# Optimization experiments

Measured on AMD Instinct MI355X. Metric: run time of the kernel, lower is better.

Reference implementation:

```python
import math
import jax, jax.numpy as jnp
import numpy as np

B, S, HID = 2, 2048, 3072
NH, HD = 32, 96            # num_heads, head_dim; num_kv_heads == num_heads (n_rep = 1)
OP = NH * HD + 2 * (NH * HD)  # 9216


def _rope_tables(seq_len, head_dim, theta=10000.0):
    inv_freq = 1.0 / (theta ** (np.arange(0, head_dim, 2, dtype=np.float32) / head_dim))
    t = np.arange(seq_len, dtype=np.float32)
    freqs = np.outer(t, inv_freq)                      # [S, HD/2]
    emb = np.concatenate([freqs, freqs], axis=-1)      # [S, HD]
    return jnp.asarray(np.cos(emb)), jnp.asarray(np.sin(emb))


def setup_inputs() -> dict:
    key = jax.random.key(0)
    k1, k2, k3 = jax.random.split(key, 3)
    hidden_states = jax.random.normal(k1, (B, S, HID), dtype=jnp.float32)
    cos, sin = _rope_tables(S, HD)
    # additive causal mask [B, 1, S, S]
    neg = jnp.finfo(jnp.float32).min
    causal = jnp.where(jnp.tril(jnp.ones((S, S), dtype=bool)), 0.0, neg)
    attention_mask = jnp.broadcast_to(causal[None, None], (B, 1, S, S)).astype(jnp.float32)
    Wqkv = jax.random.normal(k2, (HID, OP), dtype=jnp.float32) * (HID ** -0.5)
    Wo = jax.random.normal(k3, (NH * HD, HID), dtype=jnp.float32) * ((NH * HD) ** -0.5)
    return {"hidden_states": hidden_states, "cos": cos, "sin": sin,
            "attention_mask": attention_mask, "Wqkv": Wqkv, "Wo": Wo}


def _rotate_half(x):
    x1, x2 = jnp.split(x, 2, axis=-1)
    return jnp.concatenate([-x2, x1], axis=-1)


def reference(hidden_states, cos, sin, attention_mask, Wqkv, Wo):
    bsz, q_len, _ = hidden_states.shape
    qkv = hidden_states @ Wqkv                                    # [B,S,OP]
    q, k, v = jnp.split(qkv, [NH * HD, 2 * NH * HD], axis=-1)
    # [B,S,H*D] -> [B,H,S,D]
    to_bhsd = lambda t: t.reshape(bsz, q_len, NH, HD).transpose(0, 2, 1, 3)
    q, k, v = to_bhsd(q), to_bhsd(k), to_bhsd(v)
    c = cos[None, None]                                           # [1,1,S,D]
    s = sin[None, None]
    q = q * c + _rotate_half(q) * s
    k = k * c + _rotate_half(k) * s
    # num_key_value_groups == 1, so repeat_kv is identity.
    scores = jnp.einsum('bhqd,bhkd->bhqk', q, k) / math.sqrt(HD)  # [B,H,S,S]
    scores = scores + attention_mask
    attn = jax.nn.softmax(scores.astype(jnp.float32), axis=-1).astype(v.dtype)
    # dropout p=0.0 / eval -> identity
    out = jnp.einsum('bhqk,bhkd->bhqd', attn, v)                  # [B,H,S,D]
    out = out.transpose(0, 2, 1, 3).reshape(bsz, q_len, NH * HD)
    return out @ Wo                                               # [B,S,HID]
```

## Files before the change

### kernel.cpp

```cpp
#include <hip/hip_runtime.h>

typedef __bf16  bf16x8 __attribute__((ext_vector_type(8)));
typedef float   f32x4  __attribute__((ext_vector_type(4)));
typedef short   i16x8  __attribute__((ext_vector_type(8)));
typedef unsigned short u16x4 __attribute__((ext_vector_type(4)));

__device__ __forceinline__ float bf2f(unsigned short u) {
    union { unsigned int i; float f; } v; v.i = ((unsigned int)u) << 16; return v.f;
}
__device__ __forceinline__ unsigned short f2bf(float f) {
    union { float f; unsigned int i; } v; v.f = f;
    unsigned int r = v.i + 0x7FFFu + ((v.i >> 16) & 1u);
    return (unsigned short)(r >> 16);
}
__device__ __forceinline__ void gload_lds16(const void* g, void* l) {
    __builtin_amdgcn_global_load_lds(
        (const __attribute__((address_space(1))) void*)g,
        (__attribute__((address_space(3))) void*)l, 16, 0, 0);
}

__global__ __launch_bounds__(256) void cast_f32_bf16(
    const float* __restrict__ in, unsigned short* __restrict__ out, int n8)
{
    int i = blockIdx.x * 256 + threadIdx.x;
    if (i >= n8) return;
    const f32x4* p = (const f32x4*)(in + (long)i * 8);
    f32x4 a = p[0], b = p[1];
    i16x8 o;
    o[0]=(short)f2bf(a[0]); o[1]=(short)f2bf(a[1]); o[2]=(short)f2bf(a[2]); o[3]=(short)f2bf(a[3]);
    o[4]=(short)f2bf(b[0]); o[5]=(short)f2bf(b[1]); o[6]=(short)f2bf(b[2]); o[7]=(short)f2bf(b[3]);
    *(i16x8*)(out + (long)i * 8) = o;
}

__global__ __launch_bounds__(256) void transpose_cast(
    const float* __restrict__ in, unsigned short* __restrict__ out, int R, int C)
{
    __shared__ float tile[64][65];
    int c0 = blockIdx.x * 64, r0 = blockIdx.y * 64;
    int tx = threadIdx.x & 63, ty = threadIdx.x >> 6;
#pragma unroll
    for (int i = 0; i < 64; i += 4)
        tile[ty + i][tx] = in[(long)(r0 + ty + i) * C + c0 + tx];
    __syncthreads();
#pragma unroll
    for (int i = 0; i < 64; i += 4)
        out[(long)(c0 + ty + i) * R + r0 + tx] = f2bf(tile[tx][ty + i]);
}

template <int MODE>
__global__ __launch_bounds__(256) void gemm_bt(
    const unsigned short* __restrict__ A, const unsigned short* __restrict__ B,
    int K, int N,
    unsigned short* __restrict__ Qo, unsigned short* __restrict__ Ko,
    unsigned short* __restrict__ Vo, float* __restrict__ Cf)
{
    __shared__ unsigned short Al[128 * 64];
    __shared__ unsigned short Bl[128 * 64];
    const int t = threadIdx.x;
    const int w = t >> 6, l = t & 63, lhi = l >> 4, llo = l & 15;
    const int m0 = blockIdx.x * 128, n0 = blockIdx.y * 128;
    const int wmo = (w >> 1) << 6, wno = (w & 1) << 6;

    const unsigned short* ag[4];
    const unsigned short* bg[4];
#pragma unroll
    for (int i = 0; i < 4; ++i) {
        int j = i * 256 + t;
        int row = j >> 3;
        int c = (j & 7) ^ (row & 7);
        ag[i] = A + (long)(m0 + row) * K + c * 8;
        bg[i] = B + (long)(n0 + row) * K + c * 8;
    }

    f32x4 acc[4][4] = {};
    const int nkt = K >> 6;
    for (int kt = 0; kt < nkt; ++kt) {
        __syncthreads();
#pragma unroll
        for (int i = 0; i < 4; ++i) {
            gload_lds16(ag[i] + kt * 64, &Al[(i * 256 + (w << 6)) * 8]);
            gload_lds16(bg[i] + kt * 64, &Bl[(i * 256 + (w << 6)) * 8]);
        }
        __syncthreads();
#pragma unroll
        for (int kf = 0; kf < 2; ++kf) {
            bf16x8 af[4], bfv[4];
#pragma unroll
            for (int mi = 0; mi < 4; ++mi) {
                int row = wmo + mi * 16 + llo;
                int cc = (kf * 4 + lhi) ^ (row & 7);
                af[mi] = __builtin_bit_cast(bf16x8, *(const i16x8*)&Al[row * 64 + cc * 8]);
            }
#pragma unroll
            for (int ni = 0; ni < 4; ++ni) {
                int row = wno + ni * 16 + llo;
                int cc = (kf * 4 + lhi) ^ (row & 7);
                bfv[ni] = __builtin_bit_cast(bf16x8, *(const i16x8*)&Bl[row * 64 + cc * 8]);
            }
#pragma unroll
            for (int mi = 0; mi < 4; ++mi)
#pragma unroll
                for (int ni = 0; ni < 4; ++ni)
                    acc[mi][ni] = __builtin_amdgcn_mfma_f32_16x16x32_bf16(
                        af[mi], bfv[ni], acc[mi][ni], 0, 0, 0);
        }
    }

#pragma unroll
    for (int mi = 0; mi < 4; ++mi) {
        int s0g = m0 + wmo + mi * 16 + (lhi << 2);
#pragma unroll
        for (int ni = 0; ni < 4; ++ni) {
            int gcol = n0 + wno + ni * 16 + llo;
            if (MODE == 1) {
#pragma unroll
                for (int r = 0; r < 4; ++r)
                    Cf[(long)(s0g + r) * N + gcol] = acc[mi][ni][r];
            } else {
                int seg = gcol / 3072;
                int cc2 = gcol - seg * 3072;
                int h = cc2 / 96, d = cc2 - h * 96;
                int b = s0g >> 11, s = s0g & 2047;
                long bh = (long)((b << 5) + h);
                if (seg == 2) {
                    u16x4 pv;
#pragma unroll
                    for (int r = 0; r < 4; ++r) pv[r] = f2bf(acc[mi][ni][r]);
                    *(u16x4*)(Vo + (bh * 96 + d) * 2048 + s) = pv;
                } else {
                    unsigned short* dst = seg ? Ko : Qo;
#pragma unroll
                    for (int r = 0; r < 4; ++r)
                        dst[(bh * 2048 + s + r) * 96 + d] = f2bf(acc[mi][ni][r]);
                }
            }
        }
    }
}

__global__ __launch_bounds__(256) void rope_kernel(
    unsigned short* __restrict__ Qb, unsigned short* __restrict__ Kb,
    const float* __restrict__ cosT, const float* __restrict__ sinT)
{
    int i = blockIdx.x * 256 + threadIdx.x;
    int d6 = i % 6;
    int sbh = i / 6;
    int s = sbh & 2047;
    long base = (long)sbh * 96 + d6 * 8;
    const f32x4* cp = (const f32x4*)(cosT + s * 96 + d6 * 8);
    const f32x4* sp = (const f32x4*)(sinT + s * 96 + d6 * 8);
    f32x4 c0 = cp[0], c1 = cp[1], s0 = sp[0], s1 = sp[1];
    float cv[8] = {c0[0],c0[1],c0[2],c0[3],c1[0],c1[1],c1[2],c1[3]};
    float sv[8] = {s0[0],s0[1],s0[2],s0[3],s1[0],s1[1],s1[2],s1[3]};
    i16x8 qlo = *(i16x8*)(Qb + base), qhi = *(i16x8*)(Qb + base + 48);
    i16x8 klo = *(i16x8*)(Kb + base), khi = *(i16x8*)(Kb + base + 48);
    i16x8 qlo2, qhi2, klo2, khi2;
#pragma unroll
    for (int j = 0; j < 8; ++j) {
        float ql = bf2f((unsigned short)qlo[j]), qh = bf2f((unsigned short)qhi[j]);
        float kl = bf2f((unsigned short)klo[j]), kh = bf2f((unsigned short)khi[j]);
        qlo2[j] = (short)f2bf(ql * cv[j] - qh * sv[j]);
        qhi2[j] = (short)f2bf(qh * cv[j] + ql * sv[j]);
        klo2[j] = (short)f2bf(kl * cv[j] - kh * sv[j]);
        khi2[j] = (short)f2bf(kh * cv[j] + kl * sv[j]);
    }
    *(i16x8*)(Qb + base) = qlo2; *(i16x8*)(Qb + base + 48) = qhi2;
    *(i16x8*)(Kb + base) = klo2; *(i16x8*)(Kb + base + 48) = khi2;
}

__global__ __launch_bounds__(256, 3) void attn_fwd(
    const unsigned short* __restrict__ Q, const unsigned short* __restrict__ Kt,
    const unsigned short* __restrict__ Vg, unsigned short* __restrict__ O)
{
    __shared__ unsigned short Kl[64 * 104];
    __shared__ unsigned short Vl[96 * 72];
    __shared__ unsigned short Pl[4][16 * 88];
    const int t = threadIdx.x;
    const int w = t >> 6, l = t & 63, lhi = l >> 4, llo = l & 15;
    const int bx = blockIdx.x, bh = blockIdx.y;
    constexpr float C2 = 0.14724450f;

    int klds[3], vlds[3];
    const unsigned short* kg[3];
    const unsigned short* vg[3];
#pragma unroll
    for (int i = 0; i < 3; ++i) {
        int c = t + i * 256;
        int srow = c / 12, scc = c % 12;
        kg[i] = Kt + ((long)bh * 2048 + srow) * 96 + scc * 8;
        klds[i] = srow * 104 + scc * 8;
        int vrow = c >> 3, vch = c & 7;
        vg[i] = Vg + ((long)bh * 96 + vrow) * 2048 + vch * 8;
        vlds[i] = vrow * 72 + vch * 8;
    }

    const int b = bh >> 5, h = bh & 31;

    for (int pass = 0; pass < 2; ++pass) {
        const int qb = pass ? (31 - bx) : bx;
        const int q0 = qb << 6;

        bf16x8 qf[3];
        {
            const unsigned short* qp =
                Q + ((long)bh * 2048 + q0 + (w << 4) + llo) * 96 + (lhi << 3);
#pragma unroll
            for (int kf = 0; kf < 3; ++kf)
                qf[kf] = __builtin_bit_cast(bf16x8, *(const i16x8*)(qp + kf * 32));
        }

        f32x4 oacc[6] = {};
        float m_r[4] = {-1e30f, -1e30f, -1e30f, -1e30f};
        float l_l[4] = {0.f, 0.f, 0.f, 0.f};

        i16x8 kreg[3], vreg[3];
#pragma unroll
        for (int i = 0; i < 3; ++i) {
            kreg[i] = *(const i16x8*)kg[i];
            vreg[i] = *(const i16x8*)vg[i];
        }

        for (int kt = 0; kt <= qb; ++kt) {
            __syncthreads();
#pragma unroll
            for (int i = 0; i < 3; ++i) {
                *(i16x8*)&Kl[klds[i]] = kreg[i];
                *(i16x8*)&Vl[vlds[i]] = vreg[i];
            }
            __syncthreads();
            if (kt < qb) {
#pragma unroll
                for (int i = 0; i < 3; ++i) {
                    kreg[i] = *(const i16x8*)(kg[i] + (long)(kt + 1) * 64 * 96);
                    vreg[i] = *(const i16x8*)(vg[i] + (kt + 1) * 64);
                }
            }

            f32x4 sa[4] = {};
#pragma unroll
            for (int kf = 0; kf < 3; ++kf) {
#pragma unroll
                for (int nf = 0; nf < 4; ++nf) {
                    bf16x8 bfr = __builtin_bit_cast(bf16x8,
                        *(const i16x8*)&Kl[(nf * 16 + llo) * 104 + kf * 32 + (lhi << 3)]);
                    sa[nf] = __builtin_amdgcn_mfma_f32_16x16x32_bf16(qf[kf], bfr, sa[nf], 0, 0, 0);
                }
            }
            if (kt == qb) {
#pragma unroll
                for (int nf = 0; nf < 4; ++nf) {
                    int col = nf * 16 + llo;
#pragma unroll
                    for (int r = 0; r < 4; ++r)
                        if (col > (w << 4) + (lhi << 2) + r) sa[nf][r] = -1e30f;
                }
            }

#pragma unroll
            for (int r = 0; r < 4; ++r) {
                float mx = fmaxf(fmaxf(sa[0][r], sa[1][r]), fmaxf(sa[2][r], sa[3][r]));
                mx = fmaxf(mx, __shfl_xor(mx, 1));
                mx = fmaxf(mx, __shfl_xor(mx, 2));
                mx = fmaxf(mx, __shfl_xor(mx, 4));
                mx = fmaxf(mx, __shfl_xor(mx, 8));
                if (__any(mx > m_r[r] + 54.0f)) {
                    float mnew = fmaxf(m_r[r], mx);
                    float scl = exp2f((m_r[r] - mnew) * C2);
                    l_l[r] *= scl;
#pragma unroll
                    for (int nf = 0; nf < 6; ++nf) oacc[nf][r] *= scl;
                    m_r[r] = mnew;
                }
                float mC = m_r[r] * C2;
                float rs = 0.f;
#pragma unroll
                for (int nf = 0; nf < 4; ++nf) {
                    float p = exp2f(fmaf(sa[nf][r], C2, -mC));
                    rs += p;
                    Pl[w][((lhi << 2) + r) * 88 + nf * 16 + llo] = f2bf(p);
                }
                l_l[r] += rs;
            }

#pragma unroll
            for (int kf = 0; kf < 2; ++kf) {
                bf16x8 pa = __builtin_bit_cast(bf16x8,
                    *(const i16x8*)&Pl[w][llo * 88 + kf * 32 + (lhi << 3)]);
#pragma unroll
                for (int nf = 0; nf < 6; ++nf) {
                    bf16x8 bv = __builtin_bit_cast(bf16x8,
                        *(const i16x8*)&Vl[(nf * 16 + llo) * 72 + kf * 32 + (lhi << 3)]);
                    oacc[nf] = __builtin_amdgcn_mfma_f32_16x16x32_bf16(pa, bv, oacc[nf], 0, 0, 0);
                }
            }
        }

#pragma unroll
        for (int r = 0; r < 4; ++r) {
            float s = l_l[r];
            s += __shfl_xor(s, 1);
            s += __shfl_xor(s, 2);
            s += __shfl_xor(s, 4);
            s += __shfl_xor(s, 8);
            float inv = 1.0f / s;
            long ob = ((long)(b * 2048 + q0 + (w << 4) + (lhi << 2) + r)) * 3072 + h * 96;
#pragma unroll
            for (int nf = 0; nf < 6; ++nf)
                O[ob + nf * 16 + llo] = f2bf(oacc[nf][r] * inv);
        }
    }
}

extern "C" void kernel_launch(void* const* d_in, const int* in_sizes, int n_in,
                              void* d_out, int out_size, void* d_ws, size_t ws_size,
                              hipStream_t stream) {
    const float* hidden = (const float*)d_in[0];
    const float* cosT   = (const float*)d_in[1];
    const float* sinT   = (const float*)d_in[2];
    const float* Wqkv   = (const float*)d_in[4];
    const float* Wo     = (const float*)d_in[5];
    float* out = (float*)d_out;

    char* ws = (char*)d_ws;
    unsigned short* Ah  = (unsigned short*)ws;
    unsigned short* WqT = (unsigned short*)(ws + 25165824);
    unsigned short* Qb  = (unsigned short*)(ws + 25165824 + 56623104);
    unsigned short* Kb  = Qb + 12582912;
    unsigned short* Vb  = Kb + 12582912;

    cast_f32_bf16<<<6144, 256, 0, stream>>>(hidden, Ah, 1572864);
    transpose_cast<<<dim3(144, 48), 256, 0, stream>>>(Wqkv, WqT, 3072, 9216);
    gemm_bt<0><<<dim3(32, 72), 256, 0, stream>>>(Ah, WqT, 3072, 9216, Qb, Kb, Vb, nullptr);
    transpose_cast<<<dim3(48, 48), 256, 0, stream>>>(Wo, WqT, 3072, 3072);
    rope_kernel<<<3072, 256, 0, stream>>>(Qb, Kb, cosT, sinT);
    attn_fwd<<<dim3(16, 64), 256, 0, stream>>>(Qb, Kb, Vb, Ah);
    gemm_bt<1><<<dim3(32, 24), 256, 0, stream>>>(Ah, WqT, 3072, 3072,
                                                 nullptr, nullptr, nullptr, out);
}
```

Measured before the change: 560.6 us.

## Replace GEMM with 256x256 double-buffered tile kernel and XCD-aware block remap

Swaps the 128x128 single-buffered bf16 GEMM for a 256x256-tile, 512-thread kernel. It double-buffers LDS with global_load_lds prefetch two K-steps ahead, using vmcnt waits and split barriers, and raises MFMA priority with s_setprio. Blocks are remapped across the 8 XCDs for cache locality. The aim is to hide global-load latency and raise arithmetic intensity for the QKV and output projections, at the cost of 128KB of LDS and fewer workgroups (576 and 192), which hurts occupancy and tail balance on the smaller GEMM.

```diff
diff --git a/kernel.cpp b/kernel.cpp
--- a/kernel.cpp
+++ b/kernel.cpp
@@ -48,70 +48,110 @@
 }
 
 template <int MODE>
-__global__ __launch_bounds__(256) void gemm_bt(
+__global__ __launch_bounds__(512, 2) void gemm256(
     const unsigned short* __restrict__ A, const unsigned short* __restrict__ B,
-    int K, int N,
+    int K, int N, int nbx,
     unsigned short* __restrict__ Qo, unsigned short* __restrict__ Ko,
     unsigned short* __restrict__ Vo, float* __restrict__ Cf)
 {
-    __shared__ unsigned short Al[128 * 64];
-    __shared__ unsigned short Bl[128 * 64];
+    __shared__ __align__(16) unsigned short As[2][256 * 64];
+    __shared__ __align__(16) unsigned short Bs[2][256 * 64];
     const int t = threadIdx.x;
-    const int w = t >> 6, l = t & 63, lhi = l >> 4, llo = l & 15;
-    const int m0 = blockIdx.x * 128, n0 = blockIdx.y * 128;
-    const int wmo = (w >> 1) << 6, wno = (w & 1) << 6;
-
-    const unsigned short* ag[4];
-    const unsigned short* bg[4];
+    const int w = t >> 6, l = t & 63, lhi = (l >> 4), llo = l & 15;
+    const int wm = w >> 2, wn = w & 3;
+
+    const int nwg = gridDim.x, cpx = nwg >> 3;
+    const int wg = ((int)blockIdx.x & 7) * cpx + ((int)blockIdx.x >> 3);
+    const int bx = wg % nbx, by = wg / nbx;
+    const int m0 = bx << 8, n0 = by << 8;
+
+    const unsigned short* aG[4];
+    const unsigned short* bG[4];
+    int ldsOff[4];
 #pragma unroll
     for (int i = 0; i < 4; ++i) {
-        int j = i * 256 + t;
+        int j = i * 512 + t;
         int row = j >> 3;
         int c = (j & 7) ^ (row & 7);
-        ag[i] = A + (long)(m0 + row) * K + c * 8;
-        bg[i] = B + (long)(n0 + row) * K + c * 8;
-    }
-
-    f32x4 acc[4][4] = {};
+        aG[i] = A + (long)(m0 + row) * K + c * 8;
+        bG[i] = B + (long)(n0 + row) * K + c * 8;
+        ldsOff[i] = (i * 512 + (w << 6)) * 8;
+    }
+
     const int nkt = K >> 6;
+#pragma unroll
+    for (int i = 0; i < 4; ++i) {
+        gload_lds16(aG[i], &As[0][ldsOff[i]]);
+        gload_lds16(bG[i], &Bs[0][ldsOff[i]]);
+    }
+#pragma unroll
+    for (int i = 0; i < 4; ++i) {
+        gload_lds16(aG[i] + 64, &As[1][ldsOff[i]]);
+        gload_lds16(bG[i] + 64, &Bs[1][ldsOff[i]]);
+    }
+
+    f32x4 acc[8][4] = {};
+
     for (int kt = 0; kt < nkt; ++kt) {
-        __syncthreads();
-#pragma unroll
-        for (int i = 0; i < 4; ++i) {
-            gload_lds16(ag[i] + kt * 64, &Al[(i * 256 + (w << 6)) * 8]);
-            gload_lds16(bg[i] + kt * 64, &Bl[(i * 256 + (w << 6)) * 8]);
-        }
-        __syncthreads();
-#pragma unroll
-        for (int kf = 0; kf < 2; ++kf) {
-            bf16x8 af[4], bfv[4];
-#pragma unroll
-            for (int mi = 0; mi < 4; ++mi) {
-                int row = wmo + mi * 16 + llo;
-                int cc = (kf * 4 + lhi) ^ (row & 7);
-                af[mi] = __builtin_bit_cast(bf16x8, *(const i16x8*)&Al[row * 64 + cc * 8]);
-            }
-#pragma unroll
-            for (int ni = 0; ni < 4; ++ni) {
-                int row = wno + ni * 16 + llo;
-                int cc = (kf * 4 + lhi) ^ (row & 7);
-                bfv[ni] = __builtin_bit_cast(bf16x8, *(const i16x8*)&Bl[row * 64 + cc * 8]);
-            }
-#pragma unroll
-            for (int mi = 0; mi < 4; ++mi)
-#pragma unroll
-                for (int ni = 0; ni < 4; ++ni)
-                    acc[mi][ni] = __builtin_amdgcn_mfma_f32_16x16x32_bf16(
-                        af[mi], bfv[ni], acc[mi][ni], 0, 0, 0);
-        }
-    }
-
-#pragma unroll
-    for (int mi = 0; mi < 4; ++mi) {
-        int s0g = m0 + wmo + mi * 16 + (lhi << 2);
+        const int c = kt & 1;
+        if (kt < nkt - 1) asm volatile("s_waitcnt vmcnt(8)" ::: "memory");
+        else              asm volatile("s_waitcnt vmcnt(0)" ::: "memory");
+        __builtin_amdgcn_s_barrier();
+
+        const unsigned short* Ab = As[c];
+        const unsigned short* Bb = Bs[c];
+        bf16x8 af[8];
+#pragma unroll
+        for (int kh = 0; kh < 2; ++kh) {
+#pragma unroll
+            for (int mi = 0; mi < 8; ++mi) {
+                int row = (wm << 7) + (mi << 4) + llo;
+                int cc = ((kh << 2) + lhi) ^ (row & 7);
+                af[mi] = __builtin_bit_cast(bf16x8, *(const i16x8*)&Ab[row * 64 + cc * 8]);
+            }
+#pragma unroll
+            for (int nh = 0; nh < 2; ++nh) {
+                bf16x8 b0, b1;
+                {
+                    int row = (wn << 6) + (nh << 5) + llo;
+                    int cc = ((kh << 2) + lhi) ^ (row & 7);
+                    b0 = __builtin_bit_cast(bf16x8, *(const i16x8*)&Bb[row * 64 + cc * 8]);
+                    row += 16;
+                    cc = ((kh << 2) + lhi) ^ (row & 7);
+                    b1 = __builtin_bit_cast(bf16x8, *(const i16x8*)&Bb[row * 64 + cc * 8]);
+                }
+                const bool last = (kh == 1) && (nh == 1);
+                if (last) {
+                    asm volatile("s_waitcnt lgkmcnt(0)" ::: "memory");
+                }
+                __builtin_amdgcn_s_barrier();
+                if (last && (kt + 2 < nkt)) {
+                    const long off = (long)(kt + 2) * 64;
+#pragma unroll
+                    for (int i = 0; i < 4; ++i) {
+                        gload_lds16(aG[i] + off, &As[c][ldsOff[i]]);
+                        gload_lds16(bG[i] + off, &Bs[c][ldsOff[i]]);
+                    }
+                }
+                __builtin_amdgcn_s_setprio(1);
+#pragma unroll
+                for (int mi = 0; mi < 8; ++mi) {
+                    acc[mi][(nh << 1)]     = __builtin_amdgcn_mfma_f32_16x16x32_bf16(
+                        af[mi], b0, acc[mi][(nh << 1)], 0, 0, 0);
+                    acc[mi][(nh << 1) + 1] = __builtin_amdgcn_mfma_f32_16x16x32_bf16(
+                        af[mi], b1, acc[mi][(nh << 1) + 1], 0, 0, 0);
+                }
+                __builtin_amdgcn_s_setprio(0);
+            }
+        }
+    }
+
+#pragma unroll
+    for (int mi = 0; mi < 8; ++mi) {
+        int s0g = m0 + (wm << 7) + (mi << 4) + (lhi << 2);
 #pragma unroll
         for (int ni = 0; ni < 4; ++ni) {
-            int gcol = n0 + wno + ni * 16 + llo;
+            int gcol = n0 + (wn << 6) + (ni << 4) + llo;
             if (MODE == 1) {
 #pragma unroll
                 for (int r = 0; r < 4; ++r)
@@ -330,10 +370,10 @@
 
     cast_f32_bf16<<<6144, 256, 0, stream>>>(hidden, Ah, 1572864);
     transpose_cast<<<dim3(144, 48), 256, 0, stream>>>(Wqkv, WqT, 3072, 9216);
-    gemm_bt<0><<<dim3(32, 72), 256, 0, stream>>>(Ah, WqT, 3072, 9216, Qb, Kb, Vb, nullptr);
+    gemm256<0><<<576, 512, 0, stream>>>(Ah, WqT, 3072, 9216, 16, Qb, Kb, Vb, nullptr);
     transpose_cast<<<dim3(48, 48), 256, 0, stream>>>(Wo, WqT, 3072, 3072);
     rope_kernel<<<3072, 256, 0, stream>>>(Qb, Kb, cosT, sinT);
     attn_fwd<<<dim3(16, 64), 256, 0, stream>>>(Qb, Kb, Vb, Ah);
-    gemm_bt<1><<<dim3(32, 24), 256, 0, stream>>>(Ah, WqT, 3072, 3072,
-                                                 nullptr, nullptr, nullptr, out);
-}
+    gemm256<1><<<192, 512, 0, stream>>>(Ah, WqT, 3072, 3072, 16,
+                                        nullptr, nullptr, nullptr, out);
+}
```

Result: slower. 598.5 us (median of 2 runs) (+6.8%).

## Double attention Q-tile to 128 rows per block, two 16-row MFMA tiles per wave

Applied to the files above, without the earlier changes.

Each attention block now handles 128 query rows instead of 64, with every wave computing two 16-row sub-tiles that share the same K and V fragments read from LDS. This halves the K/V global loads and LDS staging per query row and halves the grid. The causal mask now uses global row and column indices over the last two KV tiles. In exchange, register use roughly doubles (occupancy hint lowered from 3 to 2), there are fewer blocks for load balancing, and a little extra masked work lands on the diagonal tiles.

```diff
diff --git a/kernel.cpp b/kernel.cpp
--- a/kernel.cpp
+++ b/kernel.cpp
@@ -168,13 +168,13 @@
     *(i16x8*)(Kb + base) = klo2; *(i16x8*)(Kb + base + 48) = khi2;
 }
 
-__global__ __launch_bounds__(256, 3) void attn_fwd(
+__global__ __launch_bounds__(256, 2) void attn_fwd(
     const unsigned short* __restrict__ Q, const unsigned short* __restrict__ Kt,
     const unsigned short* __restrict__ Vg, unsigned short* __restrict__ O)
 {
     __shared__ unsigned short Kl[64 * 104];
     __shared__ unsigned short Vl[96 * 72];
-    __shared__ unsigned short Pl[4][16 * 88];
+    __shared__ unsigned short Pl[4][32 * 88];
     const int t = threadIdx.x;
     const int w = t >> 6, l = t & 63, lhi = l >> 4, llo = l & 15;
     const int bx = blockIdx.x, bh = blockIdx.y;
@@ -197,21 +197,23 @@
     const int b = bh >> 5, h = bh & 31;
 
     for (int pass = 0; pass < 2; ++pass) {
-        const int qb = pass ? (31 - bx) : bx;
-        const int q0 = qb << 6;
-
-        bf16x8 qf[3];
-        {
+        const int qb = pass ? (15 - bx) : bx;
+        const int q0 = qb << 7;
+        const int nkv = 2 * qb + 2;
+
+        bf16x8 qf[2][3];
+#pragma unroll
+        for (int mi = 0; mi < 2; ++mi) {
             const unsigned short* qp =
-                Q + ((long)bh * 2048 + q0 + (w << 4) + llo) * 96 + (lhi << 3);
+                Q + ((long)bh * 2048 + q0 + (w << 5) + (mi << 4) + llo) * 96 + (lhi << 3);
 #pragma unroll
             for (int kf = 0; kf < 3; ++kf)
-                qf[kf] = __builtin_bit_cast(bf16x8, *(const i16x8*)(qp + kf * 32));
-        }
-
-        f32x4 oacc[6] = {};
-        float m_r[4] = {-1e30f, -1e30f, -1e30f, -1e30f};
-        float l_l[4] = {0.f, 0.f, 0.f, 0.f};
+                qf[mi][kf] = __builtin_bit_cast(bf16x8, *(const i16x8*)(qp + kf * 32));
+        }
+
+        f32x4 oacc[2][6] = {};
+        float m_r[2][4] = {{-1e30f,-1e30f,-1e30f,-1e30f},{-1e30f,-1e30f,-1e30f,-1e30f}};
+        float l_l[2][4] = {};
 
         i16x8 kreg[3], vreg[3];
 #pragma unroll
@@ -220,7 +222,7 @@
             vreg[i] = *(const i16x8*)vg[i];
         }
 
-        for (int kt = 0; kt <= qb; ++kt) {
+        for (int kt = 0; kt < nkv; ++kt) {
             __syncthreads();
 #pragma unroll
             for (int i = 0; i < 3; ++i) {
@@ -228,7 +230,7 @@
                 *(i16x8*)&Vl[vlds[i]] = vreg[i];
             }
             __syncthreads();
-            if (kt < qb) {
+            if (kt < nkv - 1) {
 #pragma unroll
                 for (int i = 0; i < 3; ++i) {
                     kreg[i] = *(const i16x8*)(kg[i] + (long)(kt + 1) * 64 * 96);
@@ -236,77 +238,96 @@
                 }
             }
 
-            f32x4 sa[4] = {};
+            f32x4 sa[2][4] = {};
 #pragma unroll
             for (int kf = 0; kf < 3; ++kf) {
 #pragma unroll
                 for (int nf = 0; nf < 4; ++nf) {
                     bf16x8 bfr = __builtin_bit_cast(bf16x8,
                         *(const i16x8*)&Kl[(nf * 16 + llo) * 104 + kf * 32 + (lhi << 3)]);
-                    sa[nf] = __builtin_amdgcn_mfma_f32_16x16x32_bf16(qf[kf], bfr, sa[nf], 0, 0, 0);
-                }
-            }
-            if (kt == qb) {
-#pragma unroll
-                for (int nf = 0; nf < 4; ++nf) {
-                    int col = nf * 16 + llo;
-#pragma unroll
-                    for (int r = 0; r < 4; ++r)
-                        if (col > (w << 4) + (lhi << 2) + r) sa[nf][r] = -1e30f;
-                }
-            }
-
+#pragma unroll
+                    for (int mi = 0; mi < 2; ++mi)
+                        sa[mi][nf] = __builtin_amdgcn_mfma_f32_16x16x32_bf16(
+                            qf[mi][kf], bfr, sa[mi][nf], 0, 0, 0);
+                }
+            }
+            if (kt >= 2 * qb) {
+#pragma unroll
+                for (int mi = 0; mi < 2; ++mi)
+#pragma unroll
+                    for (int nf = 0; nf < 4; ++nf) {
+                        int colg = (kt << 6) + nf * 16 + llo;
+#pragma unroll
+                        for (int r = 0; r < 4; ++r) {
+                            int rowg = q0 + (w << 5) + (mi << 4) + (lhi << 2) + r;
+                            if (colg > rowg) sa[mi][nf][r] = -1e30f;
+                        }
+                    }
+            }
+
+#pragma unroll
+            for (int mi = 0; mi < 2; ++mi)
 #pragma unroll
             for (int r = 0; r < 4; ++r) {
-                float mx = fmaxf(fmaxf(sa[0][r], sa[1][r]), fmaxf(sa[2][r], sa[3][r]));
+                float mx = fmaxf(fmaxf(sa[mi][0][r], sa[mi][1][r]),
+                                 fmaxf(sa[mi][2][r], sa[mi][3][r]));
                 mx = fmaxf(mx, __shfl_xor(mx, 1));
                 mx = fmaxf(mx, __shfl_xor(mx, 2));
                 mx = fmaxf(mx, __shfl_xor(mx, 4));
                 mx = fmaxf(mx, __shfl_xor(mx, 8));
-                if (__any(mx > m_r[r] + 54.0f)) {
-                    float mnew = fmaxf(m_r[r], mx);
-                    float scl = exp2f((m_r[r] - mnew) * C2);
-                    l_l[r] *= scl;
-#pragma unroll
-                    for (int nf = 0; nf < 6; ++nf) oacc[nf][r] *= scl;
-                    m_r[r] = mnew;
-                }
-                float mC = m_r[r] * C2;
+                if (__any(mx > m_r[mi][r] + 54.0f)) {
+                    float mnew = fmaxf(m_r[mi][r], mx);
+                    float scl = exp2f((m_r[mi][r] - mnew) * C2);
+                    l_l[mi][r] *= scl;
+#pragma unroll
+                    for (int nf = 0; nf < 6; ++nf) oacc[mi][nf][r] *= scl;
+                    m_r[mi][r] = mnew;
+                }
+                float mC = m_r[mi][r] * C2;
                 float rs = 0.f;
 #pragma unroll
                 for (int nf = 0; nf < 4; ++nf) {
-                    float p = exp2f(fmaf(sa[nf][r], C2, -mC));
+                    float p = exp2f(fmaf(sa[mi][nf][r], C2, -mC));
                     rs += p;
-                    Pl[w][((lhi << 2) + r) * 88 + nf * 16 + llo] = f2bf(p);
-                }
-                l_l[r] += rs;
+                    Pl[w][((mi << 4) + (lhi << 2) + r) * 88 + nf * 16 + llo] = f2bf(p);
+                }
+                l_l[mi][r] += rs;
             }
 
 #pragma unroll
             for (int kf = 0; kf < 2; ++kf) {
-                bf16x8 pa = __builtin_bit_cast(bf16x8,
-                    *(const i16x8*)&Pl[w][llo * 88 + kf * 32 + (lhi << 3)]);
+                bf16x8 pa[2];
+#pragma unroll
+                for (int mi = 0; mi < 2; ++mi)
+                    pa[mi] = __builtin_bit_cast(bf16x8,
+                        *(const i16x8*)&Pl[w][((mi << 4) + llo) * 88 + kf * 32 + (lhi << 3)]);
 #pragma unroll
                 for (int nf = 0; nf < 6; ++nf) {
                     bf16x8 bv = __builtin_bit_cast(bf16x8,
                         *(const i16x8*)&Vl[(nf * 16 + llo) * 72 + kf * 32 + (lhi << 3)]);
-                    oacc[nf] = __builtin_amdgcn_mfma_f32_16x16x32_bf16(pa, bv, oacc[nf], 0, 0, 0);
-                }
-            }
-        }
-
+#pragma unroll
+                    for (int mi = 0; mi < 2; ++mi)
+                        oacc[mi][nf] = __builtin_amdgcn_mfma_f32_16x16x32_bf16(
+                            pa[mi], bv, oacc[mi][nf], 0, 0, 0);
+                }
+            }
+        }
+
+#pragma unroll
+        for (int mi = 0; mi < 2; ++mi)
 #pragma unroll
         for (int r = 0; r < 4; ++r) {
-            float s = l_l[r];
+            float s = l_l[mi][r];
             s += __shfl_xor(s, 1);
             s += __shfl_xor(s, 2);
             s += __shfl_xor(s, 4);
             s += __shfl_xor(s, 8);
             float inv = 1.0f / s;
-            long ob = ((long)(b * 2048 + q0 + (w << 4) + (lhi << 2) + r)) * 3072 + h * 96;
+            long ob = ((long)(b * 2048 + q0 + (w << 5) + (mi << 4) + (lhi << 2) + r)) * 3072
+                      + h * 96;
 #pragma unroll
             for (int nf = 0; nf < 6; ++nf)
-                O[ob + nf * 16 + llo] = f2bf(oacc[nf][r] * inv);
+                O[ob + nf * 16 + llo] = f2bf(oacc[mi][nf][r] * inv);
         }
     }
 }
@@ -333,7 +354,7 @@
     gemm_bt<0><<<dim3(32, 72), 256, 0, stream>>>(Ah, WqT, 3072, 9216, Qb, Kb, Vb, nullptr);
     transpose_cast<<<dim3(48, 48), 256, 0, stream>>>(Wo, WqT, 3072, 3072);
     rope_kernel<<<3072, 256, 0, stream>>>(Qb, Kb, cosT, sinT);
-    attn_fwd<<<dim3(16, 64), 256, 0, stream>>>(Qb, Kb, Vb, Ah);
+    attn_fwd<<<dim3(8, 64), 256, 0, stream>>>(Qb, Kb, Vb, Ah);
     gemm_bt<1><<<dim3(32, 24), 256, 0, stream>>>(Ah, WqT, 3072, 3072,
                                                  nullptr, nullptr, nullptr, out);
 }
```

After: 541.7 us. 3.4% less time.

## Rewrite attention with 32x32 MFMA, register-resident P, and double-buffered async KV staging

Applied to the files above, without the earlier changes.

The attention kernel now gives each block 256 query rows, with each wave owning 64 rows. It computes S^T with 32x32x16 bf16 MFMAs and builds the P operand in registers via permlane32 swaps, so P no longer goes through LDS. K and V tiles are double-buffered in LDS, loaded with global_load_lds into XOR-swizzled layouts, and the heaviest causal blocks are scheduled first. This is meant to cut LDS traffic, synchronisation and per-tile overhead, but it raises register pressure and lowers occupancy to 2 blocks per CU. Waves whose diagonal comes early also sit idle in later tiles.

```diff
diff --git a/kernel.cpp b/kernel.cpp
--- a/kernel.cpp
+++ b/kernel.cpp
@@ -2,8 +2,10 @@
 
 typedef __bf16  bf16x8 __attribute__((ext_vector_type(8)));
 typedef float   f32x4  __attribute__((ext_vector_type(4)));
+typedef float   f32x16 __attribute__((ext_vector_type(16)));
 typedef short   i16x8  __attribute__((ext_vector_type(8)));
 typedef unsigned short u16x4 __attribute__((ext_vector_type(4)));
+typedef unsigned int   u32x4 __attribute__((ext_vector_type(4)));
 
 __device__ __forceinline__ float bf2f(unsigned short u) {
     union { unsigned int i; float f; } v; v.i = ((unsigned int)u) << 16; return v.f;
@@ -13,10 +15,28 @@
     unsigned int r = v.i + 0x7FFFu + ((v.i >> 16) & 1u);
     return (unsigned short)(r >> 16);
 }
+__device__ __forceinline__ unsigned packbf(float lo, float hi) {
+    return (unsigned)f2bf(lo) | ((unsigned)f2bf(hi) << 16);
+}
 __device__ __forceinline__ void gload_lds16(const void* g, void* l) {
     __builtin_amdgcn_global_load_lds(
         (const __attribute__((address_space(1))) void*)g,
         (__attribute__((address_space(3))) void*)l, 16, 0, 0);
+}
+__device__ __forceinline__ void pswap(unsigned &x, unsigned &y) {
+#if __has_builtin(__builtin_amdgcn_permlane32_swap)
+    auto r = __builtin_amdgcn_permlane32_swap((int)x, (int)y, false, false);
+    x = (unsigned)r[0]; y = (unsigned)r[1];
+#else
+    unsigned nx = (threadIdx.x & 32) ? (unsigned)__shfl_xor((int)y, 32) : x;
+    unsigned ny = (threadIdx.x & 32) ? y : (unsigned)__shfl_xor((int)x, 32);
+    x = nx; y = ny;
+#endif
+}
+__device__ __forceinline__ float partner_f(float v, int hi) {
+    unsigned x = __builtin_bit_cast(unsigned, v), y = x;
+    pswap(x, y);
+    return __builtin_bit_cast(float, hi ? x : y);
 }
 
 __global__ __launch_bounds__(256) void cast_f32_bf16(
@@ -168,146 +188,158 @@
     *(i16x8*)(Kb + base) = klo2; *(i16x8*)(Kb + base + 48) = khi2;
 }
 
-__global__ __launch_bounds__(256, 3) void attn_fwd(
+__global__ __launch_bounds__(256, 2) void attn_fwd(
     const unsigned short* __restrict__ Q, const unsigned short* __restrict__ Kt,
     const unsigned short* __restrict__ Vg, unsigned short* __restrict__ O)
 {
-    __shared__ unsigned short Kl[64 * 104];
-    __shared__ unsigned short Vl[96 * 72];
-    __shared__ unsigned short Pl[4][16 * 88];
+    __shared__ __align__(16) unsigned short Kl[2][64 * 128];
+    __shared__ __align__(16) unsigned short Vl[2][96 * 64];
     const int t = threadIdx.x;
-    const int w = t >> 6, l = t & 63, lhi = l >> 4, llo = l & 15;
-    const int bx = blockIdx.x, bh = blockIdx.y;
+    const int w = t >> 6, l = t & 63;
+    const int l31 = l & 31, hi = l >> 5, l7 = l & 7;
+    const int bh = blockIdx.x;
+    const int qb = 7 - (int)blockIdx.y;
+    const int q0b = qb << 8;
+    const int nkv = 4 * qb + 4;
+    const int kd = 4 * qb + w;
     constexpr float C2 = 0.14724450f;
 
-    int klds[3], vlds[3];
-    const unsigned short* kg[3];
-    const unsigned short* vg[3];
-#pragma unroll
-    for (int i = 0; i < 3; ++i) {
-        int c = t + i * 256;
-        int srow = c / 12, scc = c % 12;
-        kg[i] = Kt + ((long)bh * 2048 + srow) * 96 + scc * 8;
-        klds[i] = srow * 104 + scc * 8;
-        int vrow = c >> 3, vch = c & 7;
-        vg[i] = Vg + ((long)bh * 96 + vrow) * 2048 + vch * 8;
-        vlds[i] = vrow * 72 + vch * 8;
-    }
+    const unsigned short* Kg  = Kt + (long)bh * 2048 * 96;
+    const unsigned short* Vgb = Vg + (long)bh * 96 * 2048;
+
+#define STAGE_KV(buf, tile)                                                        \
+    {                                                                              \
+        _Pragma("unroll")                                                          \
+        for (int i_ = 0; i_ < 4; ++i_) {                                           \
+            int row_ = (w << 4) + (i_ << 2) + (l >> 4);                            \
+            gload_lds16(Kg + ((long)(tile) * 64 + row_) * 96 +                     \
+                            (((l & 15) ^ (row_ & 7)) << 3),                        \
+                        &Kl[buf][((w << 4) + (i_ << 2)) << 7]);                    \
+        }                                                                          \
+        _Pragma("unroll")                                                          \
+        for (int i_ = 0; i_ < 3; ++i_) {                                           \
+            int row_ = w * 24 + (i_ << 3) + (l >> 3);                              \
+            gload_lds16(Vgb + (long)row_ * 2048 + (tile) * 64 +                    \
+                            ((l7 ^ (row_ & 7)) << 3),                              \
+                        &Vl[buf][(w * 24 + (i_ << 3)) << 6]);                      \
+        }                                                                          \
+    }
+
+    bf16x8 qf[2][6];
+#pragma unroll
+    for (int qs = 0; qs < 2; ++qs) {
+        const unsigned short* qp =
+            Q + ((long)bh * 2048 + q0b + (w << 6) + (qs << 5) + l31) * 96 + (hi << 3);
+#pragma unroll
+        for (int ks = 0; ks < 6; ++ks)
+            qf[qs][ks] = __builtin_bit_cast(bf16x8, *(const i16x8*)(qp + ks * 16));
+    }
+
+    f32x16 oa[2][3] = {};
+    float m_r[2] = {-1e30f, -1e30f};
+    float l_r[2] = {0.f, 0.f};
+
+    STAGE_KV(0, 0);
+    __syncthreads();
+    STAGE_KV(1, 1);
+
+    for (int kt = 0; kt < nkv; ++kt) {
+        const int cb = kt & 1;
+        if (kt <= kd) {
+            bf16x8 pf[2][4];
+#pragma unroll
+            for (int qs = 0; qs < 2; ++qs) {
+                f32x16 s0 = {}, s1 = {};
+#pragma unroll
+                for (int ks = 0; ks < 6; ++ks) {
+                    bf16x8 k0 = __builtin_bit_cast(bf16x8, *(const i16x8*)
+                        &Kl[cb][(l31 << 7) + ((((ks << 1) + hi) ^ l7) << 3)]);
+                    bf16x8 k1 = __builtin_bit_cast(bf16x8, *(const i16x8*)
+                        &Kl[cb][((32 + l31) << 7) + ((((ks << 1) + hi) ^ l7) << 3)]);
+                    s0 = __builtin_amdgcn_mfma_f32_32x32x16_bf16(k0, qf[qs][ks], s0, 0, 0, 0);
+                    s1 = __builtin_amdgcn_mfma_f32_32x32x16_bf16(k1, qf[qs][ks], s1, 0, 0, 0);
+                }
+                if (kt == kd) {
+                    const int ql = (qs << 5) + l31;
+#pragma unroll
+                    for (int r = 0; r < 16; ++r) {
+                        int kvl = (r & 3) + ((r >> 2) << 3) + (hi << 2);
+                        if (kvl > ql)      s0[r] = -1e30f;
+                        if (kvl + 32 > ql) s1[r] = -1e30f;
+                    }
+                }
+                float px = s0[0];
+#pragma unroll
+                for (int r = 1; r < 16; ++r) px = fmaxf(px, s0[r]);
+#pragma unroll
+                for (int r = 0; r < 16; ++r) px = fmaxf(px, s1[r]);
+                px = fmaxf(px, partner_f(px, hi));
+                if (__any(px > m_r[qs] + 54.0f)) {
+                    float mnew = fmaxf(m_r[qs], px);
+                    float scl = exp2f((m_r[qs] - mnew) * C2);
+                    l_r[qs] *= scl;
+#pragma unroll
+                    for (int tt = 0; tt < 3; ++tt)
+#pragma unroll
+                        for (int r = 0; r < 16; ++r) oa[qs][tt][r] *= scl;
+                    m_r[qs] = mnew;
+                }
+                const float mC = m_r[qs] * C2;
+                f32x16 p0, p1;
+                float ls = 0.f;
+#pragma unroll
+                for (int r = 0; r < 16; ++r) {
+                    p0[r] = exp2f(fmaf(s0[r], C2, -mC));
+                    p1[r] = exp2f(fmaf(s1[r], C2, -mC));
+                    ls += p0[r] + p1[r];
+                }
+                l_r[qs] += ls;
+#pragma unroll
+                for (int s = 0; s < 4; ++s) {
+                    const f32x16& pv = (s >= 2) ? p1 : p0;
+                    const int bb = (s & 1) << 3;
+                    unsigned d0 = packbf(pv[bb + 0], pv[bb + 1]);
+                    unsigned d2 = packbf(pv[bb + 4], pv[bb + 5]);
+                    pswap(d0, d2);
+                    unsigned d1 = packbf(pv[bb + 2], pv[bb + 3]);
+                    unsigned d3 = packbf(pv[bb + 6], pv[bb + 7]);
+                    pswap(d1, d3);
+                    pf[qs][s] = __builtin_bit_cast(bf16x8, (u32x4){d0, d1, d2, d3});
+                }
+            }
+#pragma unroll
+            for (int s = 0; s < 4; ++s) {
+#pragma unroll
+                for (int tt = 0; tt < 3; ++tt) {
+                    bf16x8 vf = __builtin_bit_cast(bf16x8, *(const i16x8*)
+                        &Vl[cb][((tt << 5) + l31) * 64 + ((((s << 1) + hi) ^ l7) << 3)]);
+                    oa[0][tt] = __builtin_amdgcn_mfma_f32_32x32x16_bf16(vf, pf[0][s], oa[0][tt], 0, 0, 0);
+                    oa[1][tt] = __builtin_amdgcn_mfma_f32_32x32x16_bf16(vf, pf[1][s], oa[1][tt], 0, 0, 0);
+                }
+            }
+        }
+        __syncthreads();
+        if (kt + 2 < nkv) STAGE_KV(cb, kt + 2);
+    }
+#undef STAGE_KV
 
     const int b = bh >> 5, h = bh & 31;
-
-    for (int pass = 0; pass < 2; ++pass) {
-        const int qb = pass ? (31 - bx) : bx;
-        const int q0 = qb << 6;
-
-        bf16x8 qf[3];
-        {
-            const unsigned short* qp =
-                Q + ((long)bh * 2048 + q0 + (w << 4) + llo) * 96 + (lhi << 3);
-#pragma unroll
-            for (int kf = 0; kf < 3; ++kf)
-                qf[kf] = __builtin_bit_cast(bf16x8, *(const i16x8*)(qp + kf * 32));
-        }
-
-        f32x4 oacc[6] = {};
-        float m_r[4] = {-1e30f, -1e30f, -1e30f, -1e30f};
-        float l_l[4] = {0.f, 0.f, 0.f, 0.f};
-
-        i16x8 kreg[3], vreg[3];
-#pragma unroll
-        for (int i = 0; i < 3; ++i) {
-            kreg[i] = *(const i16x8*)kg[i];
-            vreg[i] = *(const i16x8*)vg[i];
-        }
-
-        for (int kt = 0; kt <= qb; ++kt) {
-            __syncthreads();
-#pragma unroll
-            for (int i = 0; i < 3; ++i) {
-                *(i16x8*)&Kl[klds[i]] = kreg[i];
-                *(i16x8*)&Vl[vlds[i]] = vreg[i];
-            }
-            __syncthreads();
-            if (kt < qb) {
-#pragma unroll
-                for (int i = 0; i < 3; ++i) {
-                    kreg[i] = *(const i16x8*)(kg[i] + (long)(kt + 1) * 64 * 96);
-                    vreg[i] = *(const i16x8*)(vg[i] + (kt + 1) * 64);
-                }
-            }
-
-            f32x4 sa[4] = {};
-#pragma unroll
-            for (int kf = 0; kf < 3; ++kf) {
-#pragma unroll
-                for (int nf = 0; nf < 4; ++nf) {
-                    bf16x8 bfr = __builtin_bit_cast(bf16x8,
-                        *(const i16x8*)&Kl[(nf * 16 + llo) * 104 + kf * 32 + (lhi << 3)]);
-                    sa[nf] = __builtin_amdgcn_mfma_f32_16x16x32_bf16(qf[kf], bfr, sa[nf], 0, 0, 0);
-                }
-            }
-            if (kt == qb) {
-#pragma unroll
-                for (int nf = 0; nf < 4; ++nf) {
-                    int col = nf * 16 + llo;
-#pragma unroll
-                    for (int r = 0; r < 4; ++r)
-                        if (col > (w << 4) + (lhi << 2) + r) sa[nf][r] = -1e30f;
-                }
-            }
-
-#pragma unroll
-            for (int r = 0; r < 4; ++r) {
-                float mx = fmaxf(fmaxf(sa[0][r], sa[1][r]), fmaxf(sa[2][r], sa[3][r]));
-                mx = fmaxf(mx, __shfl_xor(mx, 1));
-                mx = fmaxf(mx, __shfl_xor(mx, 2));
-                mx = fmaxf(mx, __shfl_xor(mx, 4));
-                mx = fmaxf(mx, __shfl_xor(mx, 8));
-                if (__any(mx > m_r[r] + 54.0f)) {
-                    float mnew = fmaxf(m_r[r], mx);
-                    float scl = exp2f((m_r[r] - mnew) * C2);
-                    l_l[r] *= scl;
-#pragma unroll
-                    for (int nf = 0; nf < 6; ++nf) oacc[nf][r] *= scl;
-                    m_r[r] = mnew;
-                }
-                float mC = m_r[r] * C2;
-                float rs = 0.f;
-#pragma unroll
-                for (int nf = 0; nf < 4; ++nf) {
-                    float p = exp2f(fmaf(sa[nf][r], C2, -mC));
-                    rs += p;
-                    Pl[w][((lhi << 2) + r) * 88 + nf * 16 + llo] = f2bf(p);
-                }
-                l_l[r] += rs;
-            }
-
-#pragma unroll
-            for (int kf = 0; kf < 2; ++kf) {
-                bf16x8 pa = __builtin_bit_cast(bf16x8,
-                    *(const i16x8*)&Pl[w][llo * 88 + kf * 32 + (lhi << 3)]);
-#pragma unroll
-                for (int nf = 0; nf < 6; ++nf) {
-                    bf16x8 bv = __builtin_bit_cast(bf16x8,
-                        *(const i16x8*)&Vl[(nf * 16 + llo) * 72 + kf * 32 + (lhi << 3)]);
-                    oacc[nf] = __builtin_amdgcn_mfma_f32_16x16x32_bf16(pa, bv, oacc[nf], 0, 0, 0);
-                }
-            }
-        }
-
-#pragma unroll
-        for (int r = 0; r < 4; ++r) {
-            float s = l_l[r];
-            s += __shfl_xor(s, 1);
-            s += __shfl_xor(s, 2);
-            s += __shfl_xor(s, 4);
-            s += __shfl_xor(s, 8);
-            float inv = 1.0f / s;
-            long ob = ((long)(b * 2048 + q0 + (w << 4) + (lhi << 2) + r)) * 3072 + h * 96;
-#pragma unroll
-            for (int nf = 0; nf < 6; ++nf)
-                O[ob + nf * 16 + llo] = f2bf(oacc[nf][r] * inv);
-        }
+#pragma unroll
+    for (int qs = 0; qs < 2; ++qs) {
+        float lt = l_r[qs] + partner_f(l_r[qs], hi);
+        float inv = 1.0f / lt;
+        const int qg = q0b + (w << 6) + (qs << 5) + l31;
+        unsigned short* ob = O + ((long)(b * 2048 + qg)) * 3072 + h * 96;
+#pragma unroll
+        for (int tt = 0; tt < 3; ++tt)
+#pragma unroll
+            for (int qd = 0; qd < 4; ++qd) {
+                u16x4 o4;
+#pragma unroll
+                for (int j = 0; j < 4; ++j)
+                    o4[j] = f2bf(oa[qs][tt][(qd << 2) + j] * inv);
+                *(u16x4*)(ob + (tt << 5) + (qd << 3) + (hi << 2)) = o4;
+            }
     }
 }
 
@@ -333,7 +365,7 @@
     gemm_bt<0><<<dim3(32, 72), 256, 0, stream>>>(Ah, WqT, 3072, 9216, Qb, Kb, Vb, nullptr);
     transpose_cast<<<dim3(48, 48), 256, 0, stream>>>(Wo, WqT, 3072, 3072);
     rope_kernel<<<3072, 256, 0, stream>>>(Qb, Kb, cosT, sinT);
-    attn_fwd<<<dim3(16, 64), 256, 0, stream>>>(Qb, Kb, Vb, Ah);
+    attn_fwd<<<dim3(64, 8), 256, 0, stream>>>(Qb, Kb, Vb, Ah);
     gemm_bt<1><<<dim3(32, 24), 256, 0, stream>>>(Ah, WqT, 3072, 3072,
                                                  nullptr, nullptr, nullptr, out);
 }
```

Result: slower. 572.0 us (+2.0%).
